# Performance work log

Hardware: AMD Instinct MI355X
Metric: run time of the kernel (lower is better)

Reference implementation:

```python
import jax, jax.numpy as jnp
import numpy as np
import math

DIM = 2048; H = 16; QR = 1536; KVR = 512; DN = 128; DR = 64; DV = 128
BS = 4; S = 1024
QK_HEAD = DN + DR  # 192


def _rms(x, w, eps=1e-6):
    v = jnp.mean(x * x, axis=-1, keepdims=True)
    return w * (x * jax.lax.rsqrt(v + eps))


def _rope_cos_sin(seq_len, dim):
    inv_freq = 1.0 / (10000.0 ** (jnp.arange(0, dim, 2, dtype=jnp.float32) / dim))
    t = jnp.arange(seq_len, dtype=jnp.float32)
    freqs = jnp.einsum('s,d->sd', t, inv_freq)
    freqs = jnp.concatenate([freqs, freqs], axis=-1)  # [S, dim]
    return jnp.cos(freqs), jnp.sin(freqs)


def _rotate_half(x):
    x1, x2 = jnp.split(x, 2, axis=-1)
    return jnp.concatenate([-x2, x1], axis=-1)


def setup_inputs() -> dict:
    key = jax.random.key(0)
    ks = jax.random.split(key, 12)
    sd = 0.02
    x = jax.random.normal(ks[0], (BS, S, DIM), dtype=jnp.float32)
    # causal additive mask [b, s, t]
    i = jnp.arange(S)
    causal = jnp.where(i[:, None] >= i[None, :], 0.0, -1e9).astype(jnp.float32)
    mask = jnp.broadcast_to(causal, (BS, S, S))
    return {
        'x': x,
        'mask': mask,
        'wq_a_w': jax.random.normal(ks[1], (QR, DIM)) * sd,
        'wq_a_b': jnp.zeros((QR,), jnp.float32),
        'q_norm_w': jnp.ones((QR,), jnp.float32),
        'wq_b_w': jax.random.normal(ks[2], (H * QK_HEAD, QR)) * sd,
        'wq_b_b': jnp.zeros((H * QK_HEAD,), jnp.float32),
        'wkv_a_w': jax.random.normal(ks[3], (KVR + DR, DIM)) * sd,
        'wkv_a_b': jnp.zeros((KVR + DR,), jnp.float32),
        'kv_norm_w': jnp.ones((KVR,), jnp.float32),
        'wkv_b_w': jax.random.normal(ks[4], (H * (DN + DV), KVR)) * sd,
        'wo_w': jax.random.normal(ks[5], (DIM, H * DV)) * sd,
        'wo_b': jnp.zeros((DIM,), jnp.float32),
    }


def reference(x, mask, wq_a_w, wq_a_b, q_norm_w, wq_b_w, wq_b_b,
              wkv_a_w, wkv_a_b, kv_norm_w, wkv_b_w, wo_w, wo_b):
    bs, seq_len, _ = x.shape
    # Q low-rank path
    q = x @ wq_a_w.T + wq_a_b                     # [b,s,QR]
    q = _rms(q, q_norm_w)
    q = q @ wq_b_w.T + wq_b_b                     # [b,s,H*192]
    q = q.reshape(bs, seq_len, H, QK_HEAD)
    q_nope, q_pe = q[..., :DN], q[..., DN:]       # [b,s,h,128], [b,s,h,64]
    # compressed KV path
    kv = x @ wkv_a_w.T + wkv_a_b                  # [b,s,KVR+64]
    c, k_pe = kv[..., :KVR], kv[..., KVR:]        # [b,s,512], [b,s,64]
    # RoPE on the rope sub-dims
    cos, sin = _rope_cos_sin(seq_len, DR)         # [s,64]
    cos4 = cos[None, :, None, :]
    sin4 = sin[None, :, None, :]
    q_pe = q_pe * cos4 + _rotate_half(q_pe) * sin4
    k_pe4 = k_pe[:, :, None, :]
    k_pe = (k_pe4 * cos4 + _rotate_half(k_pe4) * sin4)[:, :, 0, :]  # [b,s,64]
    # weight absorption: wkv_b viewed [H, DN+DV, KVR]
    wkv_b = wkv_b_w.reshape(H, DN + DV, KVR)
    q_abs = jnp.einsum('bshd,hdc->bshc', q_nope, wkv_b[:, :DN])      # [b,s,h,512]
    c_n = _rms(c, kv_norm_w)                                         # [b,t,512]
    scores = (jnp.einsum('bshc,btc->bsht', q_abs, c_n)
              + jnp.einsum('bshr,btr->bsht', q_pe, k_pe)) / math.sqrt(QK_HEAD)
    scores = scores + mask[:, :, None, :]
    scores = jax.nn.softmax(scores, axis=-1)
    o = jnp.einsum('bsht,btc->bshc', scores, c_n)                    # [b,s,h,512]
    o = jnp.einsum('bshc,hdc->bshd', o, wkv_b[:, -DV:])              # [b,s,h,128]
    o = o.reshape(bs, seq_len, H * DV)
    return o @ wo_w.T + wo_b
```

## Files before the change

### kernel.cpp

```cpp
#include <hip/hip_runtime.h>


typedef __attribute__((ext_vector_type(8))) short bf16x8;
typedef __attribute__((ext_vector_type(4))) float f32x4;
typedef __attribute__((ext_vector_type(4))) int i32x4;
typedef unsigned short ushort_t;
typedef unsigned int uint32;

typedef const __attribute__((address_space(1))) void* gas_ptr;
typedef __attribute__((address_space(3))) void* las_ptr;

#define DEV __device__ __forceinline__
#define WAITVM(N) asm volatile("s_waitcnt vmcnt(" #N ")" ::: "memory")
#define WAITLGKM0 asm volatile("s_waitcnt lgkmcnt(0)" ::: "memory")

DEV float b2f(ushort_t u) { return __uint_as_float(((uint32)u) << 16); }
DEV ushort_t f2b(float f) {
  uint32 u = __float_as_uint(f);
  return (ushort_t)((u + 0x7fffu + ((u >> 16) & 1u)) >> 16);
}
DEV uint32 pkb(float lo, float hi) { return (uint32)f2b(lo) | ((uint32)f2b(hi) << 16); }

DEV void c4seg(const float4* __restrict__ in, ushort4* __restrict__ out, int i, int n4) {
  if (i < n4) {
    float4 v = in[i];
    ushort4 o; o.x = f2b(v.x); o.y = f2b(v.y); o.z = f2b(v.z); o.w = f2b(v.w);
    out[i] = o;
  }
}
DEV void vbseg(const float* __restrict__ in, ushort_t* __restrict__ out, int i4, int dofs) {
  int c4 = i4 & 127, d = (i4 >> 7) & 127, h = i4 >> 14;
  const float4 v = *(const float4*)(in + ((long)(h * 256 + dofs + d)) * 512 + c4 * 4);
  ushort4 o; o.x = f2b(v.x); o.y = f2b(v.y); o.z = f2b(v.z); o.w = f2b(v.w);
  ((ushort4*)out)[i4] = o;
}
__global__ __launch_bounds__(256) void castall_k(
    const float* __restrict__ x, const float* __restrict__ wq_a_w,
    const float* __restrict__ wkv_a_w, const float* __restrict__ wq_b_w,
    const float* __restrict__ wo_w, const float* __restrict__ wkv_b_w,
    ushort_t* __restrict__ xb, ushort_t* __restrict__ wcomb,
    ushort_t* __restrict__ wqb, ushort_t* __restrict__ wo,
    ushort_t* __restrict__ wkvbv, ushort_t* __restrict__ wkvbn) {
  int blk = blockIdx.x, tid = threadIdx.x;
  if (blk < 8192) {
    c4seg((const float4*)x, (ushort4*)xb, blk * 256 + tid, 2097152);
  } else if (blk < 11264) {
    c4seg((const float4*)wq_a_w, (ushort4*)wcomb, (blk - 8192) * 256 + tid, 786432);
  } else if (blk < 12416) {
    c4seg((const float4*)wkv_a_w, (ushort4*)(wcomb + 1536 * 2048),
          (blk - 11264) * 256 + tid, 294912);
  } else if (blk < 17024) {
    c4seg((const float4*)wq_b_w, (ushort4*)wqb, (blk - 12416) * 256 + tid, 1179648);
  } else if (blk < 21120) {
    c4seg((const float4*)wo_w, (ushort4*)wo, (blk - 17024) * 256 + tid, 1048576);
  } else if (blk < 22144) {
    vbseg(wkv_b_w, wkvbv, (blk - 21120) * 256 + tid, 128);
  } else {
    vbseg(wkv_b_w, wkvbn, (blk - 22144) * 256 + tid, 0);
  }
}

__global__ __launch_bounds__(512) void rmskv_k(const float* __restrict__ qa_in,
                                               ushort_t* __restrict__ qan,
                                               const float* __restrict__ q_norm_w,
                                               const float* __restrict__ kvf,
                                               const float* __restrict__ kv_norm_w,
                                               ushort_t* __restrict__ kcat,
                                               ushort_t* __restrict__ vtp,
                                               ushort_t* __restrict__ kabs) {
  __shared__ float sbuf[8];
  __shared__ ushort_t sh[8 * 512];
  int blk = blockIdx.x, tid = threadIdx.x;
  int wv = tid >> 6, lane = tid & 63;
  if (blk < 4096) {
    long row = blk;
    const float* p = qa_in + row * 1536;
    float v0 = p[tid], v1 = p[tid + 512], v2 = p[tid + 1024];
    float ss = v0 * v0 + v1 * v1 + v2 * v2;
#pragma unroll
    for (int d = 1; d <= 32; d <<= 1) ss += __shfl_xor(ss, d);
    if (lane == 0) sbuf[wv] = ss;
    __syncthreads();
    float tot = 0.f;
#pragma unroll
    for (int i = 0; i < 8; ++i) tot += sbuf[i];
    float sc = rsqrtf(tot * (1.0f / 1536.0f) + 1e-6f);
    qan[row * 1536 + tid] = f2b(v0 * sc * q_norm_w[tid]);
    qan[row * 1536 + tid + 512] = f2b(v1 * sc * q_norm_w[tid + 512]);
    qan[row * 1536 + tid + 1024] = f2b(v2 * sc * q_norm_w[tid + 1024]);
  } else {
    int kb = blk - 4096;
    long row = (long)kb * 8 + wv;
    const float* p = kvf + row * 576;
    float4 v0 = *(const float4*)(p + lane * 8);
    float4 v1 = *(const float4*)(p + lane * 8 + 4);
    float ss = v0.x * v0.x + v0.y * v0.y + v0.z * v0.z + v0.w * v0.w
             + v1.x * v1.x + v1.y * v1.y + v1.z * v1.z + v1.w * v1.w;
#pragma unroll
    for (int d = 1; d <= 32; d <<= 1) ss += __shfl_xor(ss, d);
    float sc = rsqrtf(ss * (1.0f / 512.0f) + 1e-6f);
    float4 w0 = *(const float4*)(kv_norm_w + lane * 8);
    float4 w1 = *(const float4*)(kv_norm_w + lane * 8 + 4);
    ushort_t tmp[8];
    tmp[0] = f2b(v0.x * sc * w0.x); tmp[1] = f2b(v0.y * sc * w0.y);
    tmp[2] = f2b(v0.z * sc * w0.z); tmp[3] = f2b(v0.w * sc * w0.w);
    tmp[4] = f2b(v1.x * sc * w1.x); tmp[5] = f2b(v1.y * sc * w1.y);
    tmp[6] = f2b(v1.z * sc * w1.z); tmp[7] = f2b(v1.w * sc * w1.w);
    *(uint4*)(kcat + row * 576 + lane * 8) = *(uint4*)tmp;
    *(uint4*)(sh + wv * 512 + lane * 8) = *(uint4*)tmp;
    if (lane < 32) {
      int t = (int)(row & 1023);
      float x1 = p[512 + lane], x2 = p[544 + lane];
      float ang = (float)t * powf(10000.0f, -(float)lane * (1.0f / 32.0f));
      float s, c; sincosf(ang, &s, &c);
      ushort_t r1 = f2b(x1 * c - x2 * s), r2 = f2b(x2 * c + x1 * s);
      kcat[row * 576 + 512 + lane] = r1;
      kcat[row * 576 + 544 + lane] = r2;
#pragma unroll
      for (int h = 0; h < 16; ++h) {
        long base = ((long)h * 4096 + row) * 192;
        kabs[base + 128 + lane] = r1;
        kabs[base + 160 + lane] = r2;
      }
    }
    __syncthreads();
    ushort_t t8[8];
#pragma unroll
    for (int j = 0; j < 8; ++j) t8[j] = sh[j * 512 + tid];
    int b = kb >> 7, tb = kb & 127;
    *(uint4*)(vtp + (((long)b * 128 + tb) * 512 + tid) * 8) = *(uint4*)t8;
  }
}

template <bool OUT_BF16>
__global__ __launch_bounds__(256) void gemm_bt_k(
    const ushort_t* __restrict__ A, int lda, long sAz,
    const ushort_t* __restrict__ B, int ldb, long sBz,
    void* __restrict__ C, int ldc, long sCz,
    const float* __restrict__ bias, float scale,
    int M, int N, int K) {
  __shared__ ushort_t As[2 * 4096];
  __shared__ ushort_t Bs[2 * 4096];
  int tid = threadIdx.x;
  int wave = tid >> 6, lane = tid & 63;
  int row0 = blockIdx.x * 128, col0 = blockIdx.y * 128;
  int z = blockIdx.z;
  const ushort_t* Az = A + (long)z * sAz;
  const ushort_t* Bz = B + (long)z * sBz;
  int wr = wave >> 1, wc = wave & 1;
  int lr = lane & 15, kq = lane >> 4;

  f32x4 acc[4][4];
#pragma unroll
  for (int m = 0; m < 4; ++m)
#pragma unroll
    for (int n = 0; n < 4; ++n) acc[m][n] = (f32x4){0.f, 0.f, 0.f, 0.f};

  auto stage = [&](int buf, int k0) {
#pragma unroll
    for (int rnd = 0; rnd < 2; ++rnd) {
      int e = rnd * 2048 + wave * 512 + lane * 8;
      int tr = e >> 5, tc = e & 31;
      int ar = row0 + tr; if (ar >= M) ar = M - 1;
      int br = col0 + tr; if (br >= N) br = N - 1;
      __builtin_amdgcn_global_load_lds((gas_ptr)(Az + (long)ar * lda + (k0 + tc)),
          (las_ptr)(As + buf * 4096 + rnd * 2048 + wave * 512), 16, 0, 0);
      __builtin_amdgcn_global_load_lds((gas_ptr)(Bz + (long)br * ldb + (k0 + tc)),
          (las_ptr)(Bs + buf * 4096 + rnd * 2048 + wave * 512), 16, 0, 0);
    }
  };

  stage(0, 0);
  int nk = K >> 5;
  for (int kt = 0; kt < nk; ++kt) {
    int cur = kt & 1;
    if (kt + 1 < nk) { stage(cur ^ 1, (kt + 1) * 32); WAITVM(4); }
    else { WAITVM(0); }
    __builtin_amdgcn_s_barrier();
    __builtin_amdgcn_sched_barrier(0);
    const ushort_t* Ac = As + cur * 4096;
    const ushort_t* Bc = Bs + cur * 4096;
    bf16x8 a[4], bb[4];
#pragma unroll
    for (int m = 0; m < 4; ++m)
      a[m] = *(const bf16x8*)(Ac + (wr * 64 + m * 16 + lr) * 32 + kq * 8);
#pragma unroll
    for (int n = 0; n < 4; ++n)
      bb[n] = *(const bf16x8*)(Bc + (wc * 64 + n * 16 + lr) * 32 + kq * 8);
#pragma unroll
    for (int m = 0; m < 4; ++m)
#pragma unroll
      for (int n = 0; n < 4; ++n)
        acc[m][n] = __builtin_amdgcn_mfma_f32_16x16x32_bf16(bb[n], a[m], acc[m][n], 0, 0, 0);
    __builtin_amdgcn_s_barrier();
  }

#pragma unroll
  for (int m = 0; m < 4; ++m) {
    int gr = row0 + wr * 64 + m * 16 + lr;
    if (gr >= M) continue;
#pragma unroll
    for (int n = 0; n < 4; ++n) {
      int cb = col0 + wc * 64 + n * 16 + kq * 4;
      if (cb >= N) continue;
      f32x4 v = acc[m][n];
#pragma unroll
      for (int r = 0; r < 4; ++r) v[r] = v[r] * scale + (bias ? bias[cb + r] : 0.f);
      long ci = (long)z * sCz + (long)gr * ldc + cb;
      if constexpr (OUT_BF16) {
        ushort4 pk; pk.x = f2b(v[0]); pk.y = f2b(v[1]); pk.z = f2b(v[2]); pk.w = f2b(v[3]);
        *(ushort4*)((ushort_t*)C + ci) = pk;
      } else {
        *(f32x4*)((float*)C + ci) = v;
      }
    }
  }
}

template <int MODE>
__global__ __launch_bounds__(256) void gemm64_k(
    const ushort_t* __restrict__ A, int lda,
    const ushort_t* __restrict__ B, int ldb,
    void* __restrict__ C, int ldc,
    const float* __restrict__ bias,
    void* __restrict__ C2, const float* __restrict__ bias2,
    int M, int N, int K) {
  __shared__ ushort_t As[2 * 8192];
  __shared__ ushort_t Bs[2 * 8192];
  int tid = threadIdx.x;
  int wave = tid >> 6, lane = tid & 63;
  int bid = blockIdx.y * gridDim.x + blockIdx.x;
  int nwg = gridDim.x * gridDim.y;
  int swz = (bid & 7) * (nwg >> 3) + (bid >> 3);
  int bx = swz % gridDim.x, by = swz / gridDim.x;
  int row0 = bx * 128, col0 = by * 128;
  int wr = wave >> 1, wc = wave & 1;
  int lr = lane & 15, kq = lane >> 4;
  int rsw = lr & 7;

  f32x4 acc[4][4];
#pragma unroll
  for (int m = 0; m < 4; ++m)
#pragma unroll
    for (int n = 0; n < 4; ++n) acc[m][n] = (f32x4){0.f, 0.f, 0.f, 0.f};

  auto stage = [&](int buf, int k0) {
#pragma unroll
    for (int ii = 0; ii < 4; ++ii) {
      int e = ii * 256 + tid;
      int r = e >> 3, c = e & 7;
      int scol = ((c ^ (r & 7)) << 3);
      int ar = row0 + r; if (ar >= M) ar = M - 1;
      int br = col0 + r; if (br >= N) br = N - 1;
      __builtin_amdgcn_global_load_lds((gas_ptr)(A + (long)ar * lda + k0 + scol),
          (las_ptr)(As + buf * 8192 + e * 8), 16, 0, 0);
      __builtin_amdgcn_global_load_lds((gas_ptr)(B + (long)br * ldb + k0 + scol),
          (las_ptr)(Bs + buf * 8192 + e * 8), 16, 0, 0);
    }
  };

  stage(0, 0);
  int nk = K >> 6;
  for (int kt = 0; kt < nk; ++kt) {
    int cur = kt & 1;
    if (kt + 1 < nk) { stage(cur ^ 1, (kt + 1) * 64); WAITVM(8); }
    else { WAITVM(0); }
    __builtin_amdgcn_s_barrier();
    __builtin_amdgcn_sched_barrier(0);
    const ushort_t* Ac = As + cur * 8192;
    const ushort_t* Bc = Bs + cur * 8192;
#pragma unroll
    for (int ks = 0; ks < 2; ++ks) {
      bf16x8 a[4], bb[4];
#pragma unroll
      for (int m = 0; m < 4; ++m) {
        int row = wr * 64 + m * 16 + lr;
        a[m] = *(const bf16x8*)(Ac + row * 64 + ((((ks << 2) | kq) ^ rsw) << 3));
      }
#pragma unroll
      for (int n = 0; n < 4; ++n) {
        int row = wc * 64 + n * 16 + lr;
        bb[n] = *(const bf16x8*)(Bc + row * 64 + ((((ks << 2) | kq) ^ rsw) << 3));
      }
#pragma unroll
      for (int m = 0; m < 4; ++m)
#pragma unroll
        for (int n = 0; n < 4; ++n)
          acc[m][n] = __builtin_amdgcn_mfma_f32_16x16x32_bf16(bb[n], a[m], acc[m][n], 0, 0, 0);
    }
    __builtin_amdgcn_s_barrier();
  }

  if constexpr (MODE == 0) {
#pragma unroll
    for (int m = 0; m < 4; ++m) {
      int gr = row0 + wr * 64 + m * 16 + lr;
      if (gr >= M) continue;
#pragma unroll
      for (int n = 0; n < 4; ++n) {
        int cb = col0 + wc * 64 + n * 16 + kq * 4;
        if (cb >= N) continue;
        f32x4 v = acc[m][n];
#pragma unroll
        for (int r = 0; r < 4; ++r) v[r] += bias[cb + r];
        *(f32x4*)((float*)C + (long)gr * ldc + cb) = v;
      }
    }
  } else if constexpr (MODE == 1) {
#pragma unroll
    for (int m = 0; m < 4; ++m) {
      int gr = row0 + wr * 64 + m * 16 + lr;
      if (gr >= M) continue;
#pragma unroll
      for (int n = 0; n < 4; ++n) {
        int cb = col0 + wc * 64 + n * 16 + kq * 4;
        if (cb >= N) continue;
        f32x4 v = acc[m][n];
        if (cb < 1536) {
#pragma unroll
          for (int r = 0; r < 4; ++r) v[r] += bias[cb + r];
          *(f32x4*)((float*)C + (long)gr * 1536 + cb) = v;
        } else {
          int c2 = cb - 1536;
#pragma unroll
          for (int r = 0; r < 4; ++r) v[r] += bias2[c2 + r];
          *(f32x4*)((float*)C2 + (long)gr * 576 + c2) = v;
        }
      }
    }
  } else {
    const float RS = 0.07216878364870322f;
#pragma unroll
    for (int n = 0; n < 4; ++n) {
      int cb = col0 + wc * 64 + n * 16 + kq * 4;
      int h = cb / 192, d0 = cb - h * 192;
      ushort_t* qh = (ushort_t*)C + (long)h * 4096 * 192;
      if (d0 < 128) {
        f32x4 bv;
#pragma unroll
        for (int r = 0; r < 4; ++r) bv[r] = bias[cb + r];
#pragma unroll
        for (int m = 0; m < 4; ++m) {
          int gr = row0 + wr * 64 + m * 16 + lr;
          f32x4 v = acc[m][n];
          ushort4 pk;
          pk.x = f2b((v[0] + bv[0]) * RS); pk.y = f2b((v[1] + bv[1]) * RS);
          pk.z = f2b((v[2] + bv[2]) * RS); pk.w = f2b((v[3] + bv[3]) * RS);
          *(ushort4*)(qh + (long)gr * 192 + d0) = pk;
        }
      } else if (d0 < 160) {
        int nn = (n < 2) ? n : 0;
        f32x4 bv1, bv2, invf;
#pragma unroll
        for (int r = 0; r < 4; ++r) {
          bv1[r] = bias[cb + r]; bv2[r] = bias[cb + 32 + r];
          invf[r] = powf(10000.0f, -(float)(d0 - 128 + r) * (1.0f / 32.0f));
        }
#pragma unroll
        for (int m = 0; m < 4; ++m) {
          int gr = row0 + wr * 64 + m * 16 + lr;
          int t = gr & 1023;
          f32x4 v1 = acc[m][nn], v2 = acc[m][nn + 2];
          ushort4 p1, p2;
#pragma unroll
          for (int r = 0; r < 4; ++r) {
            float s, c; sincosf((float)t * invf[r], &s, &c);
            float x1 = v1[r] + bv1[r], x2 = v2[r] + bv2[r];
            ((ushort_t*)&p1)[r] = f2b((x1 * c - x2 * s) * RS);
            ((ushort_t*)&p2)[r] = f2b((x2 * c + x1 * s) * RS);
          }
          *(ushort4*)(qh + (long)gr * 192 + d0) = p1;
          *(ushort4*)(qh + (long)gr * 192 + d0 + 32) = p2;
        }
      }
    }
  }
}

__global__ __launch_bounds__(512, 1) void flash7_k(const ushort_t* __restrict__ qcat2,
                                                   const ushort_t* __restrict__ kabs,
                                                   const ushort_t* __restrict__ vtp,
                                                   ushort_t* __restrict__ O) {
  __shared__ __align__(16) ushort_t SMEM[6400 + 2 * 16384];

  int tid = threadIdx.x;
  int wave = tid >> 6, lane = tid & 63;
  int lr = lane & 15, kq = lane >> 4;
  int bi = blockIdx.x;
  int jz = bi >> 6;
  int qb = (jz < 4) ? jz : 11 - jz;
  int bh = bi & 63;
  int h = bh >> 2, b = bh & 3;
  int s0 = qb * 128;
  int nt = (qb + 1) * 4;

  const ushort_t* kt = kabs + ((long)h * 4096 + b * 1024) * 192;
  const ushort_t* vt = vtp + (long)b * 524288;
  const ushort_t* qp = qcat2 + ((long)(h * 4096 + b * 1024 + s0 + wave * 16 + lr)) * 192 + kq * 8;

  auto stageK = [&](int t0) {
    const ushort_t* sb = kt + (long)t0 * 192;
#pragma unroll
    for (int ii = 0; ii < 2; ++ii) {
      int c = ii * 512 + tid;
      if (ii == 1 && tid >= 288) break;
      int t = (int)((unsigned)c / 25u);
      int r = c - t * 25;
      int rr = (r == 24) ? 0 : r;
      const ushort_t* src = sb + t * 192 + rr * 8;
      __builtin_amdgcn_global_load_lds((gas_ptr)src, (las_ptr)(SMEM + c * 8), 16, 0, 0);
    }
  };
  auto stageV = [&](int buf, int t0) {
    const ushort_t* sb = vt + (long)(t0 >> 3) * 4096;
    ushort_t* vb = SMEM + 6400 + buf * 16384;
#pragma unroll
    for (int ii = 0; ii < 4; ++ii) {
      int c0 = (ii * 8 + wave) * 64;
      const ushort_t* src = sb + (long)(c0 + lane) * 8;
      __builtin_amdgcn_global_load_lds((gas_ptr)src, (las_ptr)(vb + c0 * 8), 16, 0, 0);
    }
  };

  stageK(0); stageV(0, 0);
  bf16x8 qreg[6];
#pragma unroll
  for (int st = 0; st < 6; ++st) qreg[st] = *(const bf16x8*)(qp + st * 32);

  f32x4 o[32];
#pragma unroll
  for (int v = 0; v < 32; ++v) o[v] = (f32x4){0.f, 0.f, 0.f, 0.f};
  float m_run = -1e30f, l_run = 0.f;

  int row_g = s0 + wave * 16 + lr;
  int idx_lo = (((kq & 1) << 5) + lr) << 2;
  int idx_hi = idx_lo + 64;
  bool losel = (kq < 2);

  __syncthreads();

  for (int it = 0; it < nt; ++it) {
    int cur = it & 1;
    f32x4 sv0 = (f32x4){0.f, 0.f, 0.f, 0.f}, sv1 = sv0;
    __builtin_amdgcn_s_setprio(1);
#pragma unroll
    for (int st = 0; st < 6; ++st) {
      int off = st * 32 + kq * 8;
      bf16x8 k0 = *(const bf16x8*)(SMEM + lr * 200 + off);
      bf16x8 k1 = *(const bf16x8*)(SMEM + (16 + lr) * 200 + off);
      sv0 = __builtin_amdgcn_mfma_f32_16x16x32_bf16(k0, qreg[st], sv0, 0, 0, 0);
      sv1 = __builtin_amdgcn_mfma_f32_16x16x32_bf16(k1, qreg[st], sv1, 0, 0, 0);
    }
    __builtin_amdgcn_s_setprio(0);
    WAITLGKM0;
    __builtin_amdgcn_sched_barrier(0);
    __builtin_amdgcn_s_barrier();
    if (it + 1 < nt) { stageK((it + 1) * 32); stageV(cur ^ 1, (it + 1) * 32); }
    int t0 = it * 32;
    if (t0 >= s0) {
#pragma unroll
      for (int rr = 0; rr < 4; ++rr) {
        if (t0 + kq * 4 + rr > row_g) sv0[rr] = -1e30f;
        if (t0 + 16 + kq * 4 + rr > row_g) sv1[rr] = -1e30f;
      }
    }
    float mx = fmaxf(fmaxf(fmaxf(sv0[0], sv0[1]), fmaxf(sv0[2], sv0[3])),
                     fmaxf(fmaxf(sv1[0], sv1[1]), fmaxf(sv1[2], sv1[3])));
    mx = fmaxf(mx, __shfl_xor(mx, 16));
    mx = fmaxf(mx, __shfl_xor(mx, 32));
    float mn = (mx > m_run + 8.0f) ? mx : m_run;
    float alpha = __expf(m_run - mn);
    float p0 = __expf(sv0[0] - mn), p1 = __expf(sv0[1] - mn);
    float p2 = __expf(sv0[2] - mn), p3 = __expf(sv0[3] - mn);
    float p4 = __expf(sv1[0] - mn), p5 = __expf(sv1[1] - mn);
    float p6 = __expf(sv1[2] - mn), p7 = __expf(sv1[3] - mn);
    float psum = ((p0 + p1) + (p2 + p3)) + ((p4 + p5) + (p6 + p7));
    psum += __shfl_xor(psum, 16);
    psum += __shfl_xor(psum, 32);
    l_run = l_run * alpha + psum;
    m_run = mn;
    int u0 = (int)pkb(p0, p1), u1 = (int)pkb(p2, p3);
    int u2 = (int)pkb(p4, p5), u3 = (int)pkb(p6, p7);
    int b00 = __builtin_amdgcn_ds_bpermute(idx_lo, u0);
    int b10 = __builtin_amdgcn_ds_bpermute(idx_lo, u1);
    int b20 = __builtin_amdgcn_ds_bpermute(idx_lo, u2);
    int b30 = __builtin_amdgcn_ds_bpermute(idx_lo, u3);
    int b01 = __builtin_amdgcn_ds_bpermute(idx_hi, u0);
    int b11 = __builtin_amdgcn_ds_bpermute(idx_hi, u1);
    int b21 = __builtin_amdgcn_ds_bpermute(idx_hi, u2);
    int b31 = __builtin_amdgcn_ds_bpermute(idx_hi, u3);
    i32x4 w;
    w.x = losel ? b00 : b20; w.y = losel ? b10 : b30;
    w.z = losel ? b01 : b21; w.w = losel ? b11 : b31;
    bf16x8 pa = __builtin_bit_cast(bf16x8, w);
    float a0 = __shfl(alpha, kq * 4 + 0), a1 = __shfl(alpha, kq * 4 + 1);
    float a2 = __shfl(alpha, kq * 4 + 2), a3 = __shfl(alpha, kq * 4 + 3);
    if (__any((a0 != 1.f) | (a1 != 1.f) | (a2 != 1.f) | (a3 != 1.f))) {
      f32x4 av; av[0] = a0; av[1] = a1; av[2] = a2; av[3] = a3;
#pragma unroll
      for (int v = 0; v < 32; ++v) o[v] *= av;
    }
    const ushort_t* Vc = SMEM + 6400 + cur * 16384 + (kq * 512 + lr) * 8;
    __builtin_amdgcn_s_setprio(1);
#pragma unroll
    for (int v = 0; v < 32; ++v) {
      bf16x8 bv = *(const bf16x8*)(Vc + v * 128);
      o[v] = __builtin_amdgcn_mfma_f32_16x16x32_bf16(pa, bv, o[v], 0, 0, 0);
    }
    __builtin_amdgcn_s_setprio(0);
    WAITVM(0);
    __builtin_amdgcn_s_barrier();
  }
  float l0 = __shfl(l_run, kq * 4 + 0), l1 = __shfl(l_run, kq * 4 + 1);
  float l2 = __shfl(l_run, kq * 4 + 2), l3 = __shfl(l_run, kq * 4 + 3);
  f32x4 inv; inv[0] = 1.f / l0; inv[1] = 1.f / l1; inv[2] = 1.f / l2; inv[3] = 1.f / l3;
  ushort_t* ob = O + ((long)(h * 4096 + b * 1024 + s0 + wave * 16 + kq * 4)) * 512 + lr;
#pragma unroll
  for (int rr = 0; rr < 4; ++rr) {
    ushort_t* orow = ob + (long)rr * 512;
#pragma unroll
    for (int v = 0; v < 32; ++v) orow[v * 16] = f2b(o[v][rr] * inv[rr]);
  }
}

extern "C" void kernel_launch(void* const* d_in, const int* in_sizes, int n_in,
                              void* d_out, int out_size, void* d_ws, size_t ws_size,
                              hipStream_t stream) {
  (void)in_sizes; (void)n_in;
  const float* x         = (const float*)d_in[0];
  const float* wq_a_w    = (const float*)d_in[2];
  const float* wq_a_b    = (const float*)d_in[3];
  const float* q_norm_w  = (const float*)d_in[4];
  const float* wq_b_w    = (const float*)d_in[5];
  const float* wq_b_b    = (const float*)d_in[6];
  const float* wkv_a_w   = (const float*)d_in[7];
  const float* wkv_a_b   = (const float*)d_in[8];
  const float* kv_norm_w = (const float*)d_in[9];
  const float* wkv_b_w   = (const float*)d_in[10];
  const float* wo_w      = (const float*)d_in[11];
  const float* wo_b      = (const float*)d_in[12];

  char* ws = (char*)d_ws;
  constexpr size_t OFF_XB     = 0;
  constexpr size_t OFF_WCOMB  = 16777216;
  constexpr size_t OFF_WQB    = 25427968;
  constexpr size_t OFF_QA     = 34865152;
  constexpr size_t OFF_QAN    = 60030976;
  constexpr size_t OFF_QCAT2  = 72613888;
  constexpr size_t OFF_WKVBN  = 97779712;
  constexpr size_t OFF_WKVBV  = 99876864;
  constexpr size_t OFF_WO     = 101974016;
  constexpr size_t OFF_KVF    = 110362624;
  constexpr size_t OFF_KCAT   = 119799808;
  constexpr size_t OFF_VTP    = 124518400;
  constexpr size_t OFF_KABS   = 128712704;
  constexpr size_t OFF_O      = 153878528;
  constexpr size_t OFF_O2     = 220987392;
  constexpr size_t WS_NEED    = 237764608;
  if (ws_size < WS_NEED) {
    (void)hipMemsetAsync(d_out, 0, (size_t)out_size * sizeof(float), stream);
    return;
  }

  ushort_t* xb     = (ushort_t*)(ws + OFF_XB);
  ushort_t* wcomb  = (ushort_t*)(ws + OFF_WCOMB);
  ushort_t* wqb    = (ushort_t*)(ws + OFF_WQB);
  float*    qa     = (float*)(ws + OFF_QA);
  ushort_t* qan    = (ushort_t*)(ws + OFF_QAN);
  ushort_t* qcat2  = (ushort_t*)(ws + OFF_QCAT2);
  ushort_t* wkvbn  = (ushort_t*)(ws + OFF_WKVBN);
  ushort_t* wkvbv  = (ushort_t*)(ws + OFF_WKVBV);
  ushort_t* wo     = (ushort_t*)(ws + OFF_WO);
  float*    kvf    = (float*)(ws + OFF_KVF);
  ushort_t* kcat   = (ushort_t*)(ws + OFF_KCAT);
  ushort_t* vtp    = (ushort_t*)(ws + OFF_VTP);
  ushort_t* kabs   = (ushort_t*)(ws + OFF_KABS);
  ushort_t* Obuf   = (ushort_t*)(ws + OFF_O);
  ushort_t* o2     = (ushort_t*)(ws + OFF_O2);

  castall_k<<<23168, 256, 0, stream>>>(x, wq_a_w, wkv_a_w, wq_b_w, wo_w, wkv_b_w,
                                       xb, wcomb, wqb, wo, wkvbv, wkvbn);
  gemm64_k<1><<<dim3(32, 17), 256, 0, stream>>>(xb, 2048, wcomb, 2048,
      qa, 1536, wq_a_b, kvf, wkv_a_b, 4096, 2112, 2048);
  rmskv_k<<<4608, 512, 0, stream>>>(qa, qan, q_norm_w, kvf, kv_norm_w, kcat, vtp, kabs);
  gemm64_k<2><<<dim3(32, 24), 256, 0, stream>>>(qan, 1536, wqb, 1536,
      qcat2, 0, wq_b_b, nullptr, nullptr, 4096, 3072, 1536);
  gemm_bt_k<true><<<dim3(32, 1, 16), 256, 0, stream>>>(kcat, 576, 0,
      wkvbn, 512, (long)128 * 512, kabs, 192, (long)4096 * 192,
      nullptr, 1.f, 4096, 128, 512);
  flash7_k<<<512, 512, 0, stream>>>(qcat2, kabs, vtp, Obuf);
  gemm_bt_k<true><<<dim3(32, 1, 16), 256, 0, stream>>>(Obuf, 512, (long)4096 * 512,
      wkvbv, 512, (long)128 * 512, o2, 2048, 128, nullptr, 1.f, 4096, 128, 512);
  gemm64_k<0><<<dim3(32, 16), 256, 0, stream>>>(o2, 2048, wo, 2048,
      (float*)d_out, 2048, wo_b, nullptr, nullptr, 4096, 2048, 2048);
}
```

Before: 384.9 us.

## Unify GEMM kernels with 4-stage K pipeline and double-buffer K in flash attention

```diff
diff --git a/kernel.cpp b/kernel.cpp
--- a/kernel.cpp
+++ b/kernel.cpp
@@ -12,7 +12,6 @@
 
 #define DEV __device__ __forceinline__
 #define WAITVM(N) asm volatile("s_waitcnt vmcnt(" #N ")" ::: "memory")
-#define WAITLGKM0 asm volatile("s_waitcnt lgkmcnt(0)" ::: "memory")
 
 DEV float b2f(ushort_t u) { return __uint_as_float(((uint32)u) << 16); }
 DEV ushort_t f2b(float f) {
@@ -132,18 +131,26 @@
   }
 }
 
-template <bool OUT_BF16>
-__global__ __launch_bounds__(256) void gemm_bt_k(
+template <int MODE, bool SWZ>
+__global__ __launch_bounds__(256) void gemmU_k(
     const ushort_t* __restrict__ A, int lda, long sAz,
     const ushort_t* __restrict__ B, int ldb, long sBz,
     void* __restrict__ C, int ldc, long sCz,
     const float* __restrict__ bias, float scale,
+    void* __restrict__ C2, const float* __restrict__ bias2,
     int M, int N, int K) {
-  __shared__ ushort_t As[2 * 4096];
-  __shared__ ushort_t Bs[2 * 4096];
+  __shared__ ushort_t As[4 * 4096];
+  __shared__ ushort_t Bs[4 * 4096];
   int tid = threadIdx.x;
   int wave = tid >> 6, lane = tid & 63;
-  int row0 = blockIdx.x * 128, col0 = blockIdx.y * 128;
+  int bx = blockIdx.x, by = blockIdx.y;
+  if constexpr (SWZ) {
+    int bid = by * gridDim.x + bx;
+    int nwg = gridDim.x * gridDim.y;
+    int swz = (bid & 7) * (nwg >> 3) + (bid >> 3);
+    bx = swz % gridDim.x; by = swz / gridDim.x;
+  }
+  int row0 = bx * 128, col0 = by * 128;
   int z = blockIdx.z;
   const ushort_t* Az = A + (long)z * sAz;
   const ushort_t* Bz = B + (long)z * sBz;
@@ -170,16 +177,21 @@
     }
   };
 
+  int nk = K >> 5;
   stage(0, 0);
-  int nk = K >> 5;
+  if (nk > 1) stage(1, 32);
+  if (nk > 2) stage(2, 64);
   for (int kt = 0; kt < nk; ++kt) {
-    int cur = kt & 1;
-    if (kt + 1 < nk) { stage(cur ^ 1, (kt + 1) * 32); WAITVM(4); }
-    else { WAITVM(0); }
+    int ahead = nk - 1 - kt; if (ahead > 3) ahead = 3;
+    if (kt + 3 < nk) stage((kt + 3) & 3, (kt + 3) * 32);
+    if (ahead == 3)      { WAITVM(12); }
+    else if (ahead == 2) { WAITVM(8); }
+    else if (ahead == 1) { WAITVM(4); }
+    else                 { WAITVM(0); }
     __builtin_amdgcn_s_barrier();
     __builtin_amdgcn_sched_barrier(0);
-    const ushort_t* Ac = As + cur * 4096;
-    const ushort_t* Bc = Bs + cur * 4096;
+    const ushort_t* Ac = As + (kt & 3) * 4096;
+    const ushort_t* Bc = Bs + (kt & 3) * 4096;
     bf16x8 a[4], bb[4];
 #pragma unroll
     for (int m = 0; m < 4; ++m)
@@ -195,103 +207,7 @@
     __builtin_amdgcn_s_barrier();
   }
 
-#pragma unroll
-  for (int m = 0; m < 4; ++m) {
-    int gr = row0 + wr * 64 + m * 16 + lr;
-    if (gr >= M) continue;
-#pragma unroll
-    for (int n = 0; n < 4; ++n) {
-      int cb = col0 + wc * 64 + n * 16 + kq * 4;
-      if (cb >= N) continue;
-      f32x4 v = acc[m][n];
-#pragma unroll
-      for (int r = 0; r < 4; ++r) v[r] = v[r] * scale + (bias ? bias[cb + r] : 0.f);
-      long ci = (long)z * sCz + (long)gr * ldc + cb;
-      if constexpr (OUT_BF16) {
-        ushort4 pk; pk.x = f2b(v[0]); pk.y = f2b(v[1]); pk.z = f2b(v[2]); pk.w = f2b(v[3]);
-        *(ushort4*)((ushort_t*)C + ci) = pk;
-      } else {
-        *(f32x4*)((float*)C + ci) = v;
-      }
-    }
-  }
-}
-
-template <int MODE>
-__global__ __launch_bounds__(256) void gemm64_k(
-    const ushort_t* __restrict__ A, int lda,
-    const ushort_t* __restrict__ B, int ldb,
-    void* __restrict__ C, int ldc,
-    const float* __restrict__ bias,
-    void* __restrict__ C2, const float* __restrict__ bias2,
-    int M, int N, int K) {
-  __shared__ ushort_t As[2 * 8192];
-  __shared__ ushort_t Bs[2 * 8192];
-  int tid = threadIdx.x;
-  int wave = tid >> 6, lane = tid & 63;
-  int bid = blockIdx.y * gridDim.x + blockIdx.x;
-  int nwg = gridDim.x * gridDim.y;
-  int swz = (bid & 7) * (nwg >> 3) + (bid >> 3);
-  int bx = swz % gridDim.x, by = swz / gridDim.x;
-  int row0 = bx * 128, col0 = by * 128;
-  int wr = wave >> 1, wc = wave & 1;
-  int lr = lane & 15, kq = lane >> 4;
-  int rsw = lr & 7;
-
-  f32x4 acc[4][4];
-#pragma unroll
-  for (int m = 0; m < 4; ++m)
-#pragma unroll
-    for (int n = 0; n < 4; ++n) acc[m][n] = (f32x4){0.f, 0.f, 0.f, 0.f};
-
-  auto stage = [&](int buf, int k0) {
-#pragma unroll
-    for (int ii = 0; ii < 4; ++ii) {
-      int e = ii * 256 + tid;
-      int r = e >> 3, c = e & 7;
-      int scol = ((c ^ (r & 7)) << 3);
-      int ar = row0 + r; if (ar >= M) ar = M - 1;
-      int br = col0 + r; if (br >= N) br = N - 1;
-      __builtin_amdgcn_global_load_lds((gas_ptr)(A + (long)ar * lda + k0 + scol),
-          (las_ptr)(As + buf * 8192 + e * 8), 16, 0, 0);
-      __builtin_amdgcn_global_load_lds((gas_ptr)(B + (long)br * ldb + k0 + scol),
-          (las_ptr)(Bs + buf * 8192 + e * 8), 16, 0, 0);
-    }
-  };
-
-  stage(0, 0);
-  int nk = K >> 6;
-  for (int kt = 0; kt < nk; ++kt) {
-    int cur = kt & 1;
-    if (kt + 1 < nk) { stage(cur ^ 1, (kt + 1) * 64); WAITVM(8); }
-    else { WAITVM(0); }
-    __builtin_amdgcn_s_barrier();
-    __builtin_amdgcn_sched_barrier(0);
-    const ushort_t* Ac = As + cur * 8192;
-    const ushort_t* Bc = Bs + cur * 8192;
-#pragma unroll
-    for (int ks = 0; ks < 2; ++ks) {
-      bf16x8 a[4], bb[4];
-#pragma unroll
-      for (int m = 0; m < 4; ++m) {
-        int row = wr * 64 + m * 16 + lr;
-        a[m] = *(const bf16x8*)(Ac + row * 64 + ((((ks << 2) | kq) ^ rsw) << 3));
-      }
-#pragma unroll
-      for (int n = 0; n < 4; ++n) {
-        int row = wc * 64 + n * 16 + lr;
-        bb[n] = *(const bf16x8*)(Bc + row * 64 + ((((ks << 2) | kq) ^ rsw) << 3));
-      }
-#pragma unroll
-      for (int m = 0; m < 4; ++m)
-#pragma unroll
-        for (int n = 0; n < 4; ++n)
-          acc[m][n] = __builtin_amdgcn_mfma_f32_16x16x32_bf16(bb[n], a[m], acc[m][n], 0, 0, 0);
-    }
-    __builtin_amdgcn_s_barrier();
-  }
-
-  if constexpr (MODE == 0) {
+  if constexpr (MODE == 0 || MODE == 3) {
 #pragma unroll
     for (int m = 0; m < 4; ++m) {
       int gr = row0 + wr * 64 + m * 16 + lr;
@@ -302,8 +218,14 @@
         if (cb >= N) continue;
         f32x4 v = acc[m][n];
 #pragma unroll
-        for (int r = 0; r < 4; ++r) v[r] += bias[cb + r];
-        *(f32x4*)((float*)C + (long)gr * ldc + cb) = v;
+        for (int r = 0; r < 4; ++r) v[r] = v[r] * scale + (bias ? bias[cb + r] : 0.f);
+        long ci = (long)z * sCz + (long)gr * ldc + cb;
+        if constexpr (MODE == 3) {
+          ushort4 pk; pk.x = f2b(v[0]); pk.y = f2b(v[1]); pk.z = f2b(v[2]); pk.w = f2b(v[3]);
+          *(ushort4*)((ushort_t*)C + ci) = pk;
+        } else {
+          *(f32x4*)((float*)C + ci) = v;
+        }
       }
     }
   } else if constexpr (MODE == 1) {
@@ -377,11 +299,11 @@
   }
 }
 
-__global__ __launch_bounds__(512, 1) void flash7_k(const ushort_t* __restrict__ qcat2,
+__global__ __launch_bounds__(512, 1) void flash5_k(const ushort_t* __restrict__ qcat2,
                                                    const ushort_t* __restrict__ kabs,
                                                    const ushort_t* __restrict__ vtp,
                                                    ushort_t* __restrict__ O) {
-  __shared__ __align__(16) ushort_t SMEM[6400 + 2 * 16384];
+  __shared__ __align__(16) ushort_t SMEM[2 * 6400 + 2 * 16384];
 
   int tid = threadIdx.x;
   int wave = tid >> 6, lane = tid & 63;
@@ -398,8 +320,9 @@
   const ushort_t* vt = vtp + (long)b * 524288;
   const ushort_t* qp = qcat2 + ((long)(h * 4096 + b * 1024 + s0 + wave * 16 + lr)) * 192 + kq * 8;
 
-  auto stageK = [&](int t0) {
+  auto stageK = [&](int buf, int t0) {
     const ushort_t* sb = kt + (long)t0 * 192;
+    ushort_t* kb = SMEM + buf * 6400;
 #pragma unroll
     for (int ii = 0; ii < 2; ++ii) {
       int c = ii * 512 + tid;
@@ -408,12 +331,12 @@
       int r = c - t * 25;
       int rr = (r == 24) ? 0 : r;
       const ushort_t* src = sb + t * 192 + rr * 8;
-      __builtin_amdgcn_global_load_lds((gas_ptr)src, (las_ptr)(SMEM + c * 8), 16, 0, 0);
+      __builtin_amdgcn_global_load_lds((gas_ptr)src, (las_ptr)(kb + c * 8), 16, 0, 0);
     }
   };
   auto stageV = [&](int buf, int t0) {
     const ushort_t* sb = vt + (long)(t0 >> 3) * 4096;
-    ushort_t* vb = SMEM + 6400 + buf * 16384;
+    ushort_t* vb = SMEM + 12800 + buf * 16384;
 #pragma unroll
     for (int ii = 0; ii < 4; ++ii) {
       int c0 = (ii * 8 + wave) * 64;
@@ -422,7 +345,7 @@
     }
   };
 
-  stageK(0); stageV(0, 0);
+  stageK(0, 0); stageV(0, 0);
   bf16x8 qreg[6];
 #pragma unroll
   for (int st = 0; st < 6; ++st) qreg[st] = *(const bf16x8*)(qp + st * 32);
@@ -441,21 +364,19 @@
 
   for (int it = 0; it < nt; ++it) {
     int cur = it & 1;
+    if (it + 1 < nt) { stageK(cur ^ 1, (it + 1) * 32); stageV(cur ^ 1, (it + 1) * 32); }
+    const ushort_t* Kc = SMEM + cur * 6400;
     f32x4 sv0 = (f32x4){0.f, 0.f, 0.f, 0.f}, sv1 = sv0;
     __builtin_amdgcn_s_setprio(1);
 #pragma unroll
     for (int st = 0; st < 6; ++st) {
       int off = st * 32 + kq * 8;
-      bf16x8 k0 = *(const bf16x8*)(SMEM + lr * 200 + off);
-      bf16x8 k1 = *(const bf16x8*)(SMEM + (16 + lr) * 200 + off);
+      bf16x8 k0 = *(const bf16x8*)(Kc + lr * 200 + off);
+      bf16x8 k1 = *(const bf16x8*)(Kc + (16 + lr) * 200 + off);
       sv0 = __builtin_amdgcn_mfma_f32_16x16x32_bf16(k0, qreg[st], sv0, 0, 0, 0);
       sv1 = __builtin_amdgcn_mfma_f32_16x16x32_bf16(k1, qreg[st], sv1, 0, 0, 0);
     }
     __builtin_amdgcn_s_setprio(0);
-    WAITLGKM0;
-    __builtin_amdgcn_sched_barrier(0);
-    __builtin_amdgcn_s_barrier();
-    if (it + 1 < nt) { stageK((it + 1) * 32); stageV(cur ^ 1, (it + 1) * 32); }
     int t0 = it * 32;
     if (t0 >= s0) {
 #pragma unroll
@@ -500,7 +421,7 @@
 #pragma unroll
       for (int v = 0; v < 32; ++v) o[v] *= av;
     }
-    const ushort_t* Vc = SMEM + 6400 + cur * 16384 + (kq * 512 + lr) * 8;
+    const ushort_t* Vc = SMEM + 12800 + cur * 16384 + (kq * 512 + lr) * 8;
     __builtin_amdgcn_s_setprio(1);
 #pragma unroll
     for (int v = 0; v < 32; ++v) {
@@ -508,8 +429,7 @@
       o[v] = __builtin_amdgcn_mfma_f32_16x16x32_bf16(pa, bv, o[v], 0, 0, 0);
     }
     __builtin_amdgcn_s_setprio(0);
-    WAITVM(0);
-    __builtin_amdgcn_s_barrier();
+    __syncthreads();
   }
   float l0 = __shfl(l_run, kq * 4 + 0), l1 = __shfl(l_run, kq * 4 + 1);
   float l2 = __shfl(l_run, kq * 4 + 2), l3 = __shfl(l_run, kq * 4 + 3);
@@ -580,17 +500,18 @@
 
   castall_k<<<23168, 256, 0, stream>>>(x, wq_a_w, wkv_a_w, wq_b_w, wo_w, wkv_b_w,
                                        xb, wcomb, wqb, wo, wkvbv, wkvbn);
-  gemm64_k<1><<<dim3(32, 17), 256, 0, stream>>>(xb, 2048, wcomb, 2048,
-      qa, 1536, wq_a_b, kvf, wkv_a_b, 4096, 2112, 2048);
+  gemmU_k<1, true><<<dim3(32, 17), 256, 0, stream>>>(xb, 2048, 0, wcomb, 2048, 0,
+      qa, 1536, 0, wq_a_b, 1.f, kvf, wkv_a_b, 4096, 2112, 2048);
   rmskv_k<<<4608, 512, 0, stream>>>(qa, qan, q_norm_w, kvf, kv_norm_w, kcat, vtp, kabs);
-  gemm64_k<2><<<dim3(32, 24), 256, 0, stream>>>(qan, 1536, wqb, 1536,
-      qcat2, 0, wq_b_b, nullptr, nullptr, 4096, 3072, 1536);
-  gemm_bt_k<true><<<dim3(32, 1, 16), 256, 0, stream>>>(kcat, 576, 0,
+  gemmU_k<2, true><<<dim3(32, 24), 256, 0, stream>>>(qan, 1536, 0, wqb, 1536, 0,
+      qcat2, 0, 0, wq_b_b, 1.f, nullptr, nullptr, 4096, 3072, 1536);
+  gemmU_k<3, false><<<dim3(32, 1, 16), 256, 0, stream>>>(kcat, 576, 0,
       wkvbn, 512, (long)128 * 512, kabs, 192, (long)4096 * 192,
-      nullptr, 1.f, 4096, 128, 512);
-  flash7_k<<<512, 512, 0, stream>>>(qcat2, kabs, vtp, Obuf);
-  gemm_bt_k<true><<<dim3(32, 1, 16), 256, 0, stream>>>(Obuf, 512, (long)4096 * 512,
-      wkvbv, 512, (long)128 * 512, o2, 2048, 128, nullptr, 1.f, 4096, 128, 512);
-  gemm64_k<0><<<dim3(32, 16), 256, 0, stream>>>(o2, 2048, wo, 2048,
-      (float*)d_out, 2048, wo_b, nullptr, nullptr, 4096, 2048, 2048);
-}
+      nullptr, 1.f, nullptr, nullptr, 4096, 128, 512);
+  flash5_k<<<512, 512, 0, stream>>>(qcat2, kabs, vtp, Obuf);
+  gemmU_k<3, false><<<dim3(32, 1, 16), 256, 0, stream>>>(Obuf, 512, (long)4096 * 512,
+      wkvbv, 512, (long)128 * 512, o2, 2048, 128,
+      nullptr, 1.f, nullptr, nullptr, 4096, 128, 512);
+  gemmU_k<0, true><<<dim3(32, 16), 256, 0, stream>>>(o2, 2048, 0, wo, 2048, 0,
+      (float*)d_out, 2048, 0, wo_b, 1.f, nullptr, nullptr, 4096, 2048, 2048);
+}
```

Measured after the change: 418.0 us. 8.6% more time.
